# Performance work log

Measured on AMD Instinct MI355X. Metric: run time of the kernel, lower is better.

Reference implementation:

```python
import jax, jax.numpy as jnp
import numpy as np

N_SRC = 100000
N_DST = 100000
E = 500000
D = 128
L = 2


def _sage(x_src, x_dst, e_src, e_dst, W_self, W_neigh, b):
    # DGL SAGEConv('mean'): out = x_dst @ W_self^T + mean_neighbors(x_src) @ W_neigh^T + b
    n_dst = x_dst.shape[0]
    msg_sum = jax.ops.segment_sum(x_src[e_src], e_dst, num_segments=n_dst)  # [n_dst, D]
    deg = jax.ops.segment_sum(jnp.ones((e_dst.shape[0],), x_src.dtype), e_dst, num_segments=n_dst)
    h_neigh = msg_sum / jnp.maximum(deg, 1.0)[:, None]  # isolated nodes -> 0
    return x_dst @ W_self.T + h_neigh @ W_neigh.T + b


def setup_inputs() -> dict:
    key = jax.random.key(0)
    ks = jax.random.split(key, 10)
    s = 1.0 / np.sqrt(D)
    return {
        "x_src": jax.random.normal(ks[0], (N_SRC, D), jnp.float32),
        "x_dst": jax.random.normal(ks[1], (N_DST, D), jnp.float32),
        "e_src": jax.random.randint(ks[2], (E,), 0, N_SRC, jnp.int32),
        "e_dst": jax.random.randint(ks[3], (E,), 0, N_DST, jnp.int32),
        "W_ship_self": jax.random.normal(ks[4], (L, D, D), jnp.float32) * s,
        "W_ship_neigh": jax.random.normal(ks[5], (L, D, D), jnp.float32) * s,
        "b_ship": jnp.zeros((L, D), jnp.float32),
        "W_rev_self": jax.random.normal(ks[6], (L, D, D), jnp.float32) * s,
        "W_rev_neigh": jax.random.normal(ks[7], (L, D, D), jnp.float32) * s,
        "b_rev": jnp.zeros((L, D), jnp.float32),
    }


def reference(x_src, x_dst, e_src, e_dst, W_ship_self, W_ship_neigh, b_ship,
              W_rev_self, W_rev_neigh, b_rev):
    h_s, h_d = x_src, x_dst
    n_layers = W_ship_self.shape[0]
    for l in range(n_layers):
        # ('source','ship','destination'): messages source -> destination
        new_d = _sage(h_s, h_d, e_src, e_dst, W_ship_self[l], W_ship_neigh[l], b_ship[l])
        # ('destination','rev_ship','source'): messages destination -> source
        new_s = _sage(h_d, h_s, e_dst, e_src, W_rev_self[l], W_rev_neigh[l], b_rev[l])
        h_d = jax.nn.relu(new_d)
        h_s = jax.nn.relu(new_s)
        # dropout p=0.0 (eval) -> identity
    return h_s, h_d
```

## Files before the change

kernel.cpp:

```cpp
#include <hip/hip_runtime.h>
#include <hip/hip_bf16.h>

#define NN 100000
#define EDGES 500000
#define DD 128
#define NBKT 196
#define SLACK 3584
#define CHUNK 4096
#define BPD ((EDGES + CHUNK - 1) / CHUNK)

typedef short bf16x8 __attribute__((ext_vector_type(8)));
typedef float f32x4  __attribute__((ext_vector_type(4)));

__device__ __forceinline__ unsigned short f2bf(float f) {
    unsigned u = __float_as_uint(f);
    u += 0x7fffu + ((u >> 16) & 1u);
    return (unsigned short)(u >> 16);
}

__device__ __forceinline__ void gld_lds16(const void* g, void* l) {
    __builtin_amdgcn_global_load_lds(
        (const __attribute__((address_space(1))) unsigned int*)g,
        (__attribute__((address_space(3))) unsigned int*)l,
        16, 0, 0);
}

__global__ void f2bx_kernel(const float* __restrict__ a, const float* __restrict__ b,
                            unsigned short* __restrict__ oa, unsigned short* __restrict__ ob) {
    const float* in = blockIdx.y ? b : a;
    unsigned short* out = blockIdx.y ? ob : oa;
    int i = blockIdx.x * 256 + threadIdx.x;
    float4 v = ((const float4*)in)[i];
    ushort4 o;
    o.x = f2bf(v.x); o.y = f2bf(v.y); o.z = f2bf(v.z); o.w = f2bf(v.w);
    ((ushort4*)out)[i] = o;
}

__global__ void f2bw_kernel(const float* __restrict__ w0, const float* __restrict__ w1,
                            const float* __restrict__ w2, const float* __restrict__ w3,
                            unsigned short* __restrict__ o0, unsigned short* __restrict__ o1,
                            unsigned short* __restrict__ o2, unsigned short* __restrict__ o3) {
    const float* in; unsigned short* out;
    switch (blockIdx.y) {
        case 0: in = w0; out = o0; break;
        case 1: in = w1; out = o1; break;
        case 2: in = w2; out = o2; break;
        default: in = w3; out = o3; break;
    }
    int i = blockIdx.x * 256 + threadIdx.x;
    float4 v = ((const float4*)in)[i];
    ushort4 o;
    o.x = f2bf(v.x); o.y = f2bf(v.y); o.z = f2bf(v.z); o.w = f2bf(v.w);
    ((ushort4*)out)[i] = o;
}

__global__ __launch_bounds__(256) void bin_scatter_kernel(
    const int* __restrict__ e_src, const int* __restrict__ e_dst,
    int* __restrict__ gcnt,
    unsigned* __restrict__ recbin)
{
    const int dir = blockIdx.y;
    const int t = threadIdx.x;
    const int c0 = blockIdx.x * CHUNK;
    const int nvalid = min(CHUNK, EDGES - c0);
    const int* __restrict__ TGT = dir ? e_src : e_dst;
    const int* __restrict__ PAY = dir ? e_dst : e_src;

    __shared__ int hist[256];
    __shared__ int lbase[256];
    __shared__ int lofs[256];
    __shared__ int scanA[256], scanB[256];
    __shared__ int laddr[CHUNK];
    __shared__ unsigned lrec[CHUNK];

    hist[t] = 0;
    __syncthreads();

    int myb[16], myslot[16];
    unsigned myrec[16];
    #pragma unroll
    for (int j = 0; j < 16; ++j) {
        int e = c0 + j * 256 + t;
        myb[j] = -1;
        if (e < EDGES) {
            int tgt = TGT[e], pay = PAY[e];
            int b = tgt >> 9;
            myb[j] = b;
            myrec[j] = ((unsigned)pay << 9) | (unsigned)(tgt & 511);
            myslot[j] = atomicAdd(&hist[b], 1);
        }
    }
    __syncthreads();
    int cnt = hist[t];
    lbase[t] = (cnt > 0) ? atomicAdd(&gcnt[dir * 256 + t], cnt) : 0;
    scanA[t] = cnt;
    __syncthreads();
    int* pa = scanA; int* pb = scanB;
    for (int d = 1; d < 256; d <<= 1) {
        pb[t] = pa[t] + (t >= d ? pa[t - d] : 0);
        __syncthreads();
        int* tmp = pa; pa = pb; pb = tmp;
    }
    lofs[t] = pa[t] - cnt;
    __syncthreads();
    #pragma unroll
    for (int j = 0; j < 16; ++j) {
        if (myb[j] >= 0) {
            int b = myb[j];
            int pos = lofs[b] + myslot[j];
            int g = lbase[b] + myslot[j];
            lrec[pos] = myrec[j];
            laddr[pos] = (g < SLACK) ? (b * SLACK + g) : -1;
        }
    }
    __syncthreads();
    unsigned* __restrict__ out = recbin + (size_t)dir * NBKT * SLACK;
    #pragma unroll
    for (int j = 0; j < 16; ++j) {
        int i = j * 256 + t;
        if (i < nvalid) {
            int a = laddr[i];
            if (a >= 0) out[a] = lrec[i];
        }
    }
}

__global__ void bucket_scan_kernel(const int* __restrict__ gcnt, int* __restrict__ csr_base) {
    int t = threadIdx.x;
    __shared__ int A[256], B[256];
    for (int dir = 0; dir < 2; ++dir) {
        int c = (t < NBKT) ? min(gcnt[dir * 256 + t], SLACK) : 0;
        A[t] = c;
        __syncthreads();
        int* pa = A; int* pb = B;
        for (int d = 1; d < 256; d <<= 1) {
            pb[t] = pa[t] + (t >= d ? pa[t - d] : 0);
            __syncthreads();
            int* tmp = pa; pa = pb; pb = tmp;
        }
        if (t < NBKT) csr_base[dir * 200 + t] = pa[t] - c;
        if (t == 0)   csr_base[dir * 200 + NBKT] = pa[255];
        __syncthreads();
    }
}

__global__ __launch_bounds__(256) void fine_place_kernel(
    const unsigned* __restrict__ recbin, const int* __restrict__ gcnt,
    const int* __restrict__ csr_base,
    int* __restrict__ rp_dst, int* __restrict__ rp_src,
    float* __restrict__ inv_dst, float* __restrict__ inv_src,
    int* __restrict__ csr_dst, int* __restrict__ csr_src)
{
    const int dir = blockIdx.y;
    const int bkt = blockIdx.x;
    const int t = threadIdx.x;
    int*   __restrict__ rp  = dir ? rp_src  : rp_dst;
    float* __restrict__ inv = dir ? inv_src : inv_dst;
    int*   __restrict__ csr = dir ? csr_src : csr_dst;
    const unsigned* __restrict__ recs = recbin + ((size_t)dir * NBKT + bkt) * SLACK;
    const int cnt = min(gcnt[dir * 256 + bkt], SLACK);
    const int cbase = csr_base[dir * 200 + bkt];
    const int n0 = bkt * 512;

    __shared__ int deg[512];
    __shared__ int sA[512], sB[512];
    __shared__ int cur[512];
    deg[t] = 0; deg[t + 256] = 0;
    __syncthreads();
    for (int i = t; i < cnt; i += 256)
        atomicAdd(&deg[recs[i] & 511u], 1);
    __syncthreads();
    sA[t] = deg[t]; sA[t + 256] = deg[t + 256];
    __syncthreads();
    int* pa = sA; int* pb = sB;
    for (int d = 1; d < 512; d <<= 1) {
        pb[t]       = pa[t]       + (t >= d           ? pa[t - d]       : 0);
        pb[t + 256] = pa[t + 256] + ((t + 256) >= d   ? pa[t + 256 - d] : 0);
        __syncthreads();
        int* tmp = pa; pa = pb; pb = tmp;
    }
    #pragma unroll
    for (int k = 0; k < 2; ++k) {
        int i = t + k * 256;
        int off = pa[i] - deg[i];
        cur[i] = off;
        int node = n0 + i;
        if (node < NN) {
            rp[node] = cbase + off;
            inv[node] = 1.0f / (float)max(deg[i], 1);
        }
    }
    if (bkt == NBKT - 1 && t == 0) rp[NN] = csr_base[dir * 200 + NBKT];
    __syncthreads();
    for (int i = t; i < cnt; i += 256) {
        unsigned r = recs[i];
        int p = atomicAdd(&cur[r & 511u], 1);
        csr[cbase + p] = (int)(r >> 9);
    }
}

__global__ void aggregate2_kernel(
    const unsigned short* __restrict__ h0, const int* __restrict__ rp0,
    const int* __restrict__ csr0, const float* __restrict__ inv0, unsigned short* __restrict__ ag0,
    const unsigned short* __restrict__ h1, const int* __restrict__ rp1,
    const int* __restrict__ csr1, const float* __restrict__ inv1, unsigned short* __restrict__ ag1)
{
    const int dir = blockIdx.y;
    const unsigned short* __restrict__ h = dir ? h1 : h0;
    const int* __restrict__ rp   = dir ? rp1 : rp0;
    const int* __restrict__ csr  = dir ? csr1 : csr0;
    const float* __restrict__ inv = dir ? inv1 : inv0;
    unsigned short* __restrict__ agg = dir ? ag1 : ag0;

    int wid  = (int)((blockIdx.x * 256u + threadIdx.x) >> 6);
    int lane = threadIdx.x & 63;
    if (wid >= NN) return;
    int beg = rp[wid], end = rp[wid + 1];
    float a0 = 0.f, a1 = 0.f, b0 = 0.f, b1 = 0.f;
    int i = beg;
    for (; i + 1 < end; i += 2) {
        int c0 = csr[i], c1 = csr[i + 1];
        unsigned v0 = *(const unsigned*)(h + (size_t)c0 * DD + lane * 2);
        unsigned v1 = *(const unsigned*)(h + (size_t)c1 * DD + lane * 2);
        a0 += __uint_as_float(v0 << 16); a1 += __uint_as_float(v0 & 0xffff0000u);
        b0 += __uint_as_float(v1 << 16); b1 += __uint_as_float(v1 & 0xffff0000u);
    }
    if (i < end) {
        unsigned v = *(const unsigned*)(h + (size_t)csr[i] * DD + lane * 2);
        a0 += __uint_as_float(v << 16); a1 += __uint_as_float(v & 0xffff0000u);
    }
    float sc = inv[wid];
    a0 = (a0 + b0) * sc; a1 = (a1 + b1) * sc;
    unsigned o = (unsigned)f2bf(a0) | ((unsigned)f2bf(a1) << 16);
    *(unsigned*)(agg + (size_t)wid * DD + lane * 2) = o;
}

__global__ __launch_bounds__(256, 2) void mfma_gemm2_kernel(
    const unsigned short* __restrict__ Hs0, const unsigned short* __restrict__ Ha0,
    const unsigned short* __restrict__ Ws0, const unsigned short* __restrict__ Wn0,
    const float* __restrict__ bias0, float* __restrict__ outF0, unsigned short* __restrict__ outB0,
    const unsigned short* __restrict__ Hs1, const unsigned short* __restrict__ Ha1,
    const unsigned short* __restrict__ Ws1, const unsigned short* __restrict__ Wn1,
    const float* __restrict__ bias1, float* __restrict__ outF1, unsigned short* __restrict__ outB1,
    int M)
{
    const int dir = blockIdx.y;
    const unsigned short* __restrict__ Hself = dir ? Hs1 : Hs0;
    const unsigned short* __restrict__ Hagg  = dir ? Ha1 : Ha0;
    const unsigned short* __restrict__ Wself = dir ? Ws1 : Ws0;
    const unsigned short* __restrict__ Wneigh= dir ? Wn1 : Wn0;
    const float* __restrict__ bias = dir ? bias1 : bias0;
    float* __restrict__ outF = dir ? outF1 : outF0;
    unsigned short* __restrict__ outB = dir ? outB1 : outB0;

    __shared__ __align__(16) unsigned short sW[128 * 256];
    __shared__ __align__(16) unsigned short sA[128 * 64];
    const int tid  = threadIdx.x;
    const int lane = tid & 63;
    const int w    = tid >> 6;
    const int row0 = blockIdx.x * 128;

    {
        const int s = tid & 7;
        #pragma unroll
        for (int r = 0; r < 4; ++r) {
            int ldsrow = r * 32 + (tid >> 3);
            int c = s ^ (ldsrow & 7);
            int grow = row0 + ldsrow; if (grow >= M) grow = M - 1;
            gld_lds16(Hself + (size_t)grow * 128 + c * 8, sA + ldsrow * 64 + s * 8);
        }
    }
    #pragma unroll
    for (int i = 0; i < 16; ++i) {
        int q = i * 256 + tid;
        int n = q >> 5, c = q & 31;
        const unsigned short* src = (c < 16) ? (Wself + n * 128 + c * 8)
                                             : (Wneigh + n * 128 + (c - 16) * 8);
        int d = n * 256 + (c & 24) * 8 + (((c ^ n) & 7) * 8);
        *(uint4*)(sW + d) = *(const uint4*)src;
    }

    f32x4 acc[4][4];
    #pragma unroll
    for (int mt = 0; mt < 4; ++mt)
        #pragma unroll
        for (int nt = 0; nt < 4; ++nt) acc[mt][nt] = (f32x4){0.f, 0.f, 0.f, 0.f};

    const int mbase = (w >> 1) * 64;
    const int nbase = (w & 1) * 64;
    const int l15 = lane & 15;
    const int l4  = lane >> 4;

    __syncthreads();

    for (int chunk = 0; chunk < 4; ++chunk) {
        #pragma unroll
        for (int kl = 0; kl < 2; ++kl) {
            int ks = chunk * 2 + kl;
            bf16x8 a[4], b[4];
            #pragma unroll
            for (int mt = 0; mt < 4; ++mt) {
                int row = mbase + mt * 16 + l15;
                int cc = kl * 4 + l4;
                a[mt] = *(const bf16x8*)(sA + row * 64 + ((cc ^ (row & 7)) * 8));
            }
            #pragma unroll
            for (int nt = 0; nt < 4; ++nt) {
                int n = nbase + nt * 16 + l15;
                int c = ks * 4 + l4;
                b[nt] = *(const bf16x8*)(sW + n * 256 + (c & 24) * 8 + (((c ^ n) & 7) * 8));
            }
            #pragma unroll
            for (int mt = 0; mt < 4; ++mt)
                #pragma unroll
                for (int nt = 0; nt < 4; ++nt)
                    acc[mt][nt] = __builtin_amdgcn_mfma_f32_16x16x32_bf16(a[mt], b[nt], acc[mt][nt], 0, 0, 0);
        }
        if (chunk < 3) {
            __syncthreads();
            int nc = chunk + 1;
            const unsigned short* Hm = (nc < 2) ? Hself : Hagg;
            int colbase = (nc & 1) * 64;
            const int s = tid & 7;
            #pragma unroll
            for (int r = 0; r < 4; ++r) {
                int ldsrow = r * 32 + (tid >> 3);
                int c = s ^ (ldsrow & 7);
                int grow = row0 + ldsrow; if (grow >= M) grow = M - 1;
                gld_lds16(Hm + (size_t)grow * 128 + colbase + c * 8, sA + ldsrow * 64 + s * 8);
            }
            __syncthreads();
        }
    }

    #pragma unroll
    for (int nt = 0; nt < 4; ++nt) {
        int col = nbase + nt * 16 + l15;
        float bj = bias[col];
        #pragma unroll
        for (int mt = 0; mt < 4; ++mt) {
            #pragma unroll
            for (int r = 0; r < 4; ++r) {
                int grow = row0 + mbase + mt * 16 + l4 * 4 + r;
                if (grow < M) {
                    float v = fmaxf(acc[mt][nt][r] + bj, 0.f);
                    if (outF) outF[(size_t)grow * 128 + col] = v;
                    else      outB[(size_t)grow * 128 + col] = f2bf(v);
                }
            }
        }
    }
}

extern "C" void kernel_launch(void* const* d_in, const int* in_sizes, int n_in,
                              void* d_out, int out_size, void* d_ws, size_t ws_size,
                              hipStream_t stream) {
    const float* x_src        = (const float*)d_in[0];
    const float* x_dst        = (const float*)d_in[1];
    const int*   e_src        = (const int*)d_in[2];
    const int*   e_dst        = (const int*)d_in[3];
    const float* W_ship_self  = (const float*)d_in[4];
    const float* W_ship_neigh = (const float*)d_in[5];
    const float* b_ship       = (const float*)d_in[6];
    const float* W_rev_self   = (const float*)d_in[7];
    const float* W_rev_neigh  = (const float*)d_in[8];
    const float* b_rev        = (const float*)d_in[9];
    float* out = (float*)d_out;

    char* ws = (char*)d_ws;
    size_t off = 0;
    auto alloc = [&](size_t bytes) {
        char* p = ws + off;
        off = (off + bytes + 255) & ~(size_t)255;
        return p;
    };
    unsigned short* xs_bf = (unsigned short*)alloc((size_t)NN * DD * 2);
    unsigned short* xd_bf = (unsigned short*)alloc((size_t)NN * DD * 2);
    unsigned short* agg1  = (unsigned short*)alloc((size_t)NN * DD * 2);
    unsigned short* agg2  = (unsigned short*)alloc((size_t)NN * DD * 2);
    unsigned short* Wss_bf = (unsigned short*)alloc(2 * DD * DD * 2);
    unsigned short* Wsn_bf = (unsigned short*)alloc(2 * DD * DD * 2);
    unsigned short* Wrs_bf = (unsigned short*)alloc(2 * DD * DD * 2);
    unsigned short* Wrn_bf = (unsigned short*)alloc(2 * DD * DD * 2);
    int* gcnt = (int*)alloc(2 * 256 * 4);
    int* csr_base = (int*)alloc(2 * 200 * 4);
    unsigned* recbin = (unsigned*)alloc((size_t)2 * NBKT * SLACK * 4);
    int* rp_dst = (int*)alloc((NN + 1) * 4);
    int* rp_src = (int*)alloc((NN + 1) * 4);
    float* inv_dst = (float*)alloc(NN * 4);
    float* inv_src = (float*)alloc(NN * 4);
    int* csr_dst = (int*)alloc(EDGES * 4);
    int* csr_src = (int*)alloc(EDGES * 4);
    (void)ws_size; (void)in_sizes; (void)n_in; (void)out_size;

    hipMemsetAsync(gcnt, 0, 2 * 256 * 4, stream);

    const int xn4 = NN * DD / 4;
    f2bx_kernel<<<dim3(xn4 / 256, 2), 256, 0, stream>>>(x_src, x_dst, xs_bf, xd_bf);
    f2bw_kernel<<<dim3(32, 4), 256, 0, stream>>>(W_ship_self, W_ship_neigh, W_rev_self, W_rev_neigh,
                                                 Wss_bf, Wsn_bf, Wrs_bf, Wrn_bf);

    bin_scatter_kernel<<<dim3(BPD, 2), 256, 0, stream>>>(e_src, e_dst, gcnt, recbin);
    bucket_scan_kernel<<<1, 256, 0, stream>>>(gcnt, csr_base);
    fine_place_kernel<<<dim3(NBKT, 2), 256, 0, stream>>>(recbin, gcnt, csr_base,
        rp_dst, rp_src, inv_dst, inv_src, csr_dst, csr_src);

    float* out_s = out;
    float* out_d = out + (size_t)NN * DD;
    const int gemm_grid = (NN + 127) / 128;
    const int agg_grid  = (NN * 64 + 255) / 256;

    for (int l = 0; l < 2; ++l) {
        aggregate2_kernel<<<dim3(agg_grid, 2), 256, 0, stream>>>(
            xs_bf, rp_dst, csr_dst, inv_dst, agg1,
            xd_bf, rp_src, csr_src, inv_src, agg2);
        mfma_gemm2_kernel<<<dim3(gemm_grid, 2), 256, 0, stream>>>(
            xd_bf, agg1, Wss_bf + l * DD * DD, Wsn_bf + l * DD * DD, b_ship + l * DD,
            l ? out_d : nullptr, l ? nullptr : xd_bf,
            xs_bf, agg2, Wrs_bf + l * DD * DD, Wrn_bf + l * DD * DD, b_rev + l * DD,
            l ? out_s : nullptr, l ? nullptr : xs_bf,
            NN);
    }
}
```

Before: 509.0 us.

## Load GEMM A operands directly from global into registers with prefetch

The fused SAGE linear kernel no longer stages activation rows in LDS through async global-to-LDS copies with barriers between chunks. Each lane now loads its MFMA A fragments straight from global memory and prefetches the next k-step's A and B fragments into registers, which removes the per-chunk __syncthreads and the LDS round trip. In exchange, each 16-byte global load is scattered (16 rows per wave) and rows are re-read by the two waves sharing an M tile, and register pressure rises from double-buffered fragments.

Measured after the change: 528.4 us. +3.8%, slower.

```diff
diff --git a/kernel.cpp b/kernel.cpp
--- a/kernel.cpp
+++ b/kernel.cpp
@@ -16,13 +16,6 @@
     unsigned u = __float_as_uint(f);
     u += 0x7fffu + ((u >> 16) & 1u);
     return (unsigned short)(u >> 16);
-}
-
-__device__ __forceinline__ void gld_lds16(const void* g, void* l) {
-    __builtin_amdgcn_global_load_lds(
-        (const __attribute__((address_space(1))) unsigned int*)g,
-        (__attribute__((address_space(3))) unsigned int*)l,
-        16, 0, 0);
 }
 
 __global__ void f2bx_kernel(const float* __restrict__ a, const float* __restrict__ b,
@@ -254,22 +247,11 @@
     unsigned short* __restrict__ outB = dir ? outB1 : outB0;
 
     __shared__ __align__(16) unsigned short sW[128 * 256];
-    __shared__ __align__(16) unsigned short sA[128 * 64];
     const int tid  = threadIdx.x;
     const int lane = tid & 63;
     const int w    = tid >> 6;
     const int row0 = blockIdx.x * 128;
 
-    {
-        const int s = tid & 7;
-        #pragma unroll
-        for (int r = 0; r < 4; ++r) {
-            int ldsrow = r * 32 + (tid >> 3);
-            int c = s ^ (ldsrow & 7);
-            int grow = row0 + ldsrow; if (grow >= M) grow = M - 1;
-            gld_lds16(Hself + (size_t)grow * 128 + c * 8, sA + ldsrow * 64 + s * 8);
-        }
-    }
     #pragma unroll
     for (int i = 0; i < 16; ++i) {
         int q = i * 256 + tid;
@@ -291,46 +273,51 @@
     const int l15 = lane & 15;
     const int l4  = lane >> 4;
 
-    __syncthreads();
-
-    for (int chunk = 0; chunk < 4; ++chunk) {
-        #pragma unroll
-        for (int kl = 0; kl < 2; ++kl) {
-            int ks = chunk * 2 + kl;
-            bf16x8 a[4], b[4];
+    const unsigned short* aps[4];
+    const unsigned short* apa[4];
+    #pragma unroll
+    for (int mt = 0; mt < 4; ++mt) {
+        int grow = row0 + mbase + mt * 16 + l15;
+        if (grow >= M) grow = M - 1;
+        aps[mt] = Hself + (size_t)grow * 128 + l4 * 8;
+        apa[mt] = Hagg  + (size_t)grow * 128 + l4 * 8;
+    }
+
+    __syncthreads();
+
+    bf16x8 a_cur[4], a_nxt[4], b_cur[4], b_nxt[4];
+    #pragma unroll
+    for (int mt = 0; mt < 4; ++mt) a_cur[mt] = *(const bf16x8*)(aps[mt]);
+    #pragma unroll
+    for (int nt = 0; nt < 4; ++nt) {
+        int n = nbase + nt * 16 + l15;
+        b_cur[nt] = *(const bf16x8*)(sW + n * 256 + (((l4 ^ n) & 7) * 8));
+    }
+
+    #pragma unroll
+    for (int ks = 0; ks < 8; ++ks) {
+        if (ks < 7) {
+            const int ks1 = ks + 1;
+            const int col = (ks1 & 3) * 32;
             #pragma unroll
-            for (int mt = 0; mt < 4; ++mt) {
-                int row = mbase + mt * 16 + l15;
-                int cc = kl * 4 + l4;
-                a[mt] = *(const bf16x8*)(sA + row * 64 + ((cc ^ (row & 7)) * 8));
-            }
+            for (int mt = 0; mt < 4; ++mt)
+                a_nxt[mt] = *(const bf16x8*)(((ks1 < 4) ? aps[mt] : apa[mt]) + col);
+            const int c1 = ks1 * 4 + l4;
             #pragma unroll
             for (int nt = 0; nt < 4; ++nt) {
                 int n = nbase + nt * 16 + l15;
-                int c = ks * 4 + l4;
-                b[nt] = *(const bf16x8*)(sW + n * 256 + (c & 24) * 8 + (((c ^ n) & 7) * 8));
+                b_nxt[nt] = *(const bf16x8*)(sW + n * 256 + (c1 & 24) * 8 + (((c1 ^ n) & 7) * 8));
             }
+        }
+        #pragma unroll
+        for (int mt = 0; mt < 4; ++mt)
             #pragma unroll
-            for (int mt = 0; mt < 4; ++mt)
-                #pragma unroll
-                for (int nt = 0; nt < 4; ++nt)
-                    acc[mt][nt] = __builtin_amdgcn_mfma_f32_16x16x32_bf16(a[mt], b[nt], acc[mt][nt], 0, 0, 0);
-        }
-        if (chunk < 3) {
-            __syncthreads();
-            int nc = chunk + 1;
-            const unsigned short* Hm = (nc < 2) ? Hself : Hagg;
-            int colbase = (nc & 1) * 64;
-            const int s = tid & 7;
-            #pragma unroll
-            for (int r = 0; r < 4; ++r) {
-                int ldsrow = r * 32 + (tid >> 3);
-                int c = s ^ (ldsrow & 7);
-                int grow = row0 + ldsrow; if (grow >= M) grow = M - 1;
-                gld_lds16(Hm + (size_t)grow * 128 + colbase + c * 8, sA + ldsrow * 64 + s * 8);
-            }
-            __syncthreads();
-        }
+            for (int nt = 0; nt < 4; ++nt)
+                acc[mt][nt] = __builtin_amdgcn_mfma_f32_16x16x32_bf16(a_cur[mt], b_cur[nt], acc[mt][nt], 0, 0, 0);
+        #pragma unroll
+        for (int mt = 0; mt < 4; ++mt) a_cur[mt] = a_nxt[mt];
+        #pragma unroll
+        for (int nt = 0; nt < 4; ++nt) b_cur[nt] = b_nxt[nt];
     }
 
     #pragma unroll
```
